# Performance work log

Hardware: AMD Instinct MI355X
Metric: run time of the kernel (lower is better)

The kernel has to match this reference:

```python
import math
import jax, jax.numpy as jnp
import numpy as np

DIM = 512
HEADS = 8
LS = 64  # local_size
SCALE = (DIM // HEADS) ** -0.5


def _normalize(x, eps=1e-12):
    # torch F.normalize(dim=-1): x / max(||x||, eps)
    n = jnp.linalg.norm(x, axis=-1, keepdims=True)
    return x / jnp.maximum(n, eps)


def setup_inputs() -> dict:
    key = jax.random.key(0)
    k0, k1, k2 = jax.random.split(key, 3)
    B, S, D = 8, 4096, DIM
    return {
        "x": jax.random.normal(k0, (B, S, D), jnp.float32),
        "W_qkv": jax.random.normal(k1, (D, 3 * D), jnp.float32) * 0.02,
        "b_qkv": jnp.zeros((3 * D,), jnp.float32),
        "W_proj": jax.random.normal(k2, (D, D), jnp.float32) * 0.02,
        "b_proj": jnp.zeros((D,), jnp.float32),
    }


def reference(x, W_qkv, b_qkv, W_proj, b_proj):
    B, S, D = x.shape
    H = HEADS
    d = D // H
    ls = LS
    nl = S // ls
    ntimes = int(math.log2(nl))

    # qkv projection -> [3, B, H, S, d]
    qkv = (x @ W_qkv + b_qkv).reshape(B, S, 3, H, d).transpose(2, 0, 3, 1, 4)
    q_pre = qkv[0].reshape(B * H, S, d).transpose(0, 2, 1)  # [BH, d, S]

    q_idx_last = jnp.broadcast_to(jnp.arange(S)[None, :], (B * H, S))

    # recursive content-based bipartition (unrolled: ntimes is static)
    for _ in range(ntimes):
        bh, dd, n = q_pre.shape
        q_avg = q_pre.reshape(bh, dd, 2, n // 2).mean(-1)        # [bh, d, 2]
        q_avg = _normalize(q_avg.transpose(0, 2, 1))             # [bh, 2, d]
        q_norm = _normalize(q_pre.transpose(0, 2, 1))            # [bh, n, d]
        # squared euclidean distance [bh, n, 2]
        sq = (jnp.sum(q_norm ** 2, -1)[:, :, None]
              + jnp.sum(q_avg ** 2, -1)[:, None, :]
              - 2.0 * jnp.einsum('bnd,bcd->bnc', q_norm, q_avg))
        q_ratio = (sq[:, :, 0] + 1.0) / (sq[:, :, 1] + 1.0)
        q_idx = jnp.argsort(q_ratio, axis=-1)                    # [bh, n]
        q_idx_last = jnp.take_along_axis(q_idx_last, q_idx, axis=-1).reshape(bh * 2, n // 2)
        q_pre = jnp.take_along_axis(q_pre, q_idx[:, None, :], axis=-1)
        # 'b d (c n) -> (b c) d n' with c=2
        q_pre = q_pre.reshape(bh, dd, 2, n // 2).transpose(0, 2, 1, 3).reshape(bh * 2, dd, n // 2)

    q_idx = q_idx_last.reshape(B, H, S)
    q_idx_rev = jnp.argsort(q_idx, axis=-1)

    # gather qkv along token dim with routed permutation
    qkv_pre = jnp.take_along_axis(qkv, q_idx[None, :, :, :, None], axis=3)  # [3,B,H,S,d]
    # 'qkv b h (nl ls) d -> qkv (b nl) h ls d'
    qkv_pre = qkv_pre.reshape(3, B, H, nl, ls, d).transpose(0, 1, 3, 2, 4, 5).reshape(3, B * nl, H, ls, d)
    q, k, v = qkv_pre[0], qkv_pre[1], qkv_pre[2]

    # windowed diff-softmax-mul attention (softmax over head dim d)
    attn = jax.nn.softmax((q - k) * SCALE, axis=-1)
    out = attn * v                                               # [(B nl), H, ls, d]

    # '(b nl) h ls d -> b h d (nl ls)'
    out = out.reshape(B, nl, H, ls, d).transpose(0, 2, 4, 1, 3).reshape(B, H, d, S)
    out = jnp.take_along_axis(out, q_idx_rev[:, :, None, :], axis=-1)
    res = out.reshape(B, D, S).transpose(0, 2, 1)                # [B, S, D]
    res = res @ W_proj + b_proj
    return x + res
```

## Files before the change

kernel.cpp:

```cpp
#include <hip/hip_runtime.h>
#include <hip/hip_bf16.h>

typedef __bf16 bf16;
typedef __attribute__((ext_vector_type(8))) __bf16 bf16x8;
typedef __attribute__((ext_vector_type(4))) __bf16 bf16x4;
typedef __attribute__((ext_vector_type(4))) float f32x4;

#define M_TOK 32768
#define D_    512
#define N_QKV 1536
#define BK    64
#define SCALE_ 0.125f

#define AS1 __attribute__((address_space(1)))
#define AS3 __attribute__((address_space(3)))

__global__ __launch_bounds__(256) void cvt_bf16(const float* __restrict__ in,
                                                bf16* __restrict__ out, int n4) {
  int i = blockIdx.x * 256 + threadIdx.x;
  if (i >= n4) return;
  f32x4 v = ((const f32x4*)in)[i];
  bf16x4 o;
  o[0] = (bf16)v[0]; o[1] = (bf16)v[1]; o[2] = (bf16)v[2]; o[3] = (bf16)v[3];
  ((bf16x4*)out)[i] = o;
}

template <int PERM>
__global__ __launch_bounds__(256) void transpose_cvt(const float* __restrict__ in,
                                                     bf16* __restrict__ out,
                                                     int K, int N) {
  __shared__ float tile[32][33];
  int n0 = blockIdx.x * 32, k0 = blockIdx.y * 32;
  int tx = threadIdx.x, ty = threadIdx.y;
  for (int i = 0; i < 32; i += 8)
    tile[ty + i][tx] = in[(size_t)(k0 + ty + i) * N + n0 + tx];
  __syncthreads();
  for (int i = 0; i < 32; i += 8) {
    int n = n0 + ty + i;
    int np = n;
    if (PERM) {
      int h = (n & 511) >> 6, qkv = n >> 9;
      np = h * 192 + qkv * 64 + (n & 63);
    }
    out[(size_t)np * K + k0 + tx] = (bf16)tile[tx][ty + i];
  }
}

__global__ __launch_bounds__(256) void gemm_qkv_softmax(const bf16* __restrict__ A,
                                                        const bf16* __restrict__ Bt,
                                                        const float* __restrict__ bqkv,
                                                        bf16* __restrict__ O) {
  __shared__ __align__(16) bf16 sA[128 * BK];
  __shared__ __align__(16) bf16 sB[192 * BK];

  const int tid = threadIdx.x;
  const int w = tid >> 6;
  const int l = tid & 63;
  const int m0 = blockIdx.x * 128;
  const int h  = blockIdx.y;
  const int n0 = h * 192;

  f32x4 acc[2][12];
#pragma unroll
  for (int i = 0; i < 2; ++i)
#pragma unroll
    for (int j = 0; j < 12; ++j) {
      f32x4 z = {0.f, 0.f, 0.f, 0.f};
      acc[i][j] = z;
    }

  const int srow = l >> 3;
  const int schunk = ((l & 7) ^ (l >> 3)) * 8;

  const int fr = l & 15;
  const int fkc = l >> 4;
  const int frs = fr & 7;

  for (int kt = 0; kt < D_; kt += BK) {
#pragma unroll
    for (int q = 0; q < 4; ++q) {
      int rowb = w * 32 + q * 8;
      const bf16* gp = A + (size_t)(m0 + rowb + srow) * D_ + kt + schunk;
      __builtin_amdgcn_global_load_lds((AS1 void*)gp, (AS3 void*)&sA[rowb * BK], 16, 0, 0);
    }
#pragma unroll
    for (int q = 0; q < 6; ++q) {
      int rowb = w * 48 + q * 8;
      const bf16* gp = Bt + (size_t)(n0 + rowb + srow) * D_ + kt + schunk;
      __builtin_amdgcn_global_load_lds((AS1 void*)gp, (AS3 void*)&sB[rowb * BK], 16, 0, 0);
    }
    __syncthreads();

#pragma unroll
    for (int kk = 0; kk < 2; ++kk) {
      const int sw = (((kk << 2) | fkc) ^ frs) * 8;
      bf16x8 af0 = *(const bf16x8*)&sA[(w * 32 + 0  + fr) * BK + sw];
      bf16x8 af1 = *(const bf16x8*)&sA[(w * 32 + 16 + fr) * BK + sw];
#pragma unroll
      for (int j = 0; j < 12; ++j) {
        bf16x8 bfj = *(const bf16x8*)&sB[(j * 16 + fr) * BK + sw];
        acc[0][j] = __builtin_amdgcn_mfma_f32_16x16x32_bf16(af0, bfj, acc[0][j], 0, 0, 0);
        acc[1][j] = __builtin_amdgcn_mfma_f32_16x16x32_bf16(af1, bfj, acc[1][j], 0, 0, 0);
      }
    }
    __syncthreads();
  }

  float bq[4], bk[4], bv[4];
#pragma unroll
  for (int jq = 0; jq < 4; ++jq) {
    int c = h * 64 + jq * 16 + fr;
    bq[jq] = bqkv[c];
    bk[jq] = bqkv[512 + c];
    bv[jq] = bqkv[1024 + c];
  }

  const int rbase = (l >> 4) * 4;
#pragma unroll
  for (int i = 0; i < 2; ++i) {
#pragma unroll
    for (int r = 0; r < 4; ++r) {
      float sc[4];
#pragma unroll
      for (int jq = 0; jq < 4; ++jq)
        sc[jq] = (acc[i][jq][r] + bq[jq] - acc[i][jq + 4][r] - bk[jq]) * SCALE_;
      float mx = fmaxf(fmaxf(sc[0], sc[1]), fmaxf(sc[2], sc[3]));
#pragma unroll
      for (int off = 1; off < 16; off <<= 1) mx = fmaxf(mx, __shfl_xor(mx, off));
      float e[4];
      float sum = 0.f;
#pragma unroll
      for (int jq = 0; jq < 4; ++jq) { e[jq] = __expf(sc[jq] - mx); sum += e[jq]; }
#pragma unroll
      for (int off = 1; off < 16; off <<= 1) sum += __shfl_xor(sum, off);
      float inv = 1.0f / sum;
      int m = m0 + w * 32 + i * 16 + rbase + r;
#pragma unroll
      for (int jq = 0; jq < 4; ++jq) {
        float o = e[jq] * inv * (acc[i][jq + 8][r] + bv[jq]);
        O[(size_t)m * D_ + h * 64 + jq * 16 + fr] = (bf16)o;
      }
    }
  }
}

__global__ __launch_bounds__(256) void gemm_bt_f32(const bf16* __restrict__ A,
                                                   const bf16* __restrict__ Bt,
                                                   const float* __restrict__ bias,
                                                   const float* __restrict__ resid,
                                                   float* __restrict__ C,
                                                   int M, int N, int K) {
  __shared__ __align__(16) bf16 sA[128 * BK];
  __shared__ __align__(16) bf16 sB[128 * BK];

  const int tid = threadIdx.x;
  const int w = tid >> 6;
  const int l = tid & 63;
  const int m0 = blockIdx.x * 128;
  const int n0 = blockIdx.y * 128;
  const int wrow = w >> 1, wcol = w & 1;

  f32x4 acc[4][4];
#pragma unroll
  for (int i = 0; i < 4; ++i)
#pragma unroll
    for (int j = 0; j < 4; ++j) {
      f32x4 z = {0.f, 0.f, 0.f, 0.f};
      acc[i][j] = z;
    }

  const int srow = l >> 3;
  const int schunk = ((l & 7) ^ (l >> 3)) * 8;
  const int fr = l & 15;
  const int fkc = l >> 4;
  const int frs = fr & 7;

  for (int kt = 0; kt < K; kt += BK) {
#pragma unroll
    for (int q = 0; q < 4; ++q) {
      int rowb = w * 32 + q * 8;
      const bf16* gp = A + (size_t)(m0 + rowb + srow) * K + kt + schunk;
      __builtin_amdgcn_global_load_lds((AS1 void*)gp, (AS3 void*)&sA[rowb * BK], 16, 0, 0);
    }
#pragma unroll
    for (int q = 0; q < 4; ++q) {
      int rowb = w * 32 + q * 8;
      const bf16* gp = Bt + (size_t)(n0 + rowb + srow) * K + kt + schunk;
      __builtin_amdgcn_global_load_lds((AS1 void*)gp, (AS3 void*)&sB[rowb * BK], 16, 0, 0);
    }
    __syncthreads();

#pragma unroll
    for (int kk = 0; kk < 2; ++kk) {
      const int sw = (((kk << 2) | fkc) ^ frs) * 8;
      bf16x8 af[4], bfr[4];
#pragma unroll
      for (int i = 0; i < 4; ++i)
        af[i] = *(const bf16x8*)&sA[(wrow * 64 + i * 16 + fr) * BK + sw];
#pragma unroll
      for (int j = 0; j < 4; ++j)
        bfr[j] = *(const bf16x8*)&sB[(wcol * 64 + j * 16 + fr) * BK + sw];
#pragma unroll
      for (int i = 0; i < 4; ++i)
#pragma unroll
        for (int j = 0; j < 4; ++j)
          acc[i][j] = __builtin_amdgcn_mfma_f32_16x16x32_bf16(af[i], bfr[j], acc[i][j], 0, 0, 0);
    }
    __syncthreads();
  }

  const int col = l & 15;
  const int rbase = (l >> 4) * 4;
#pragma unroll
  for (int j = 0; j < 4; ++j) {
    int n = n0 + wcol * 64 + j * 16 + col;
    float bv = bias[n];
#pragma unroll
    for (int i = 0; i < 4; ++i) {
#pragma unroll
      for (int r = 0; r < 4; ++r) {
        int m = m0 + wrow * 64 + i * 16 + rbase + r;
        C[(size_t)m * N + n] = acc[i][j][r] + bv + resid[(size_t)m * N + n];
      }
    }
  }
}

extern "C" void kernel_launch(void* const* d_in, const int* in_sizes, int n_in,
                              void* d_out, int out_size, void* d_ws, size_t ws_size,
                              hipStream_t stream) {
  const float* x     = (const float*)d_in[0];
  const float* Wqkv  = (const float*)d_in[1];
  const float* bqkv  = (const float*)d_in[2];
  const float* Wproj = (const float*)d_in[3];
  const float* bproj = (const float*)d_in[4];
  float* out = (float*)d_out;

  char* ws = (char*)d_ws;
  bf16* Wq_t = (bf16*)ws;
  bf16* Wp_t = (bf16*)(ws + (size_t)N_QKV * D_ * 2);
  char* p = ws + (size_t)N_QKV * D_ * 2 + (size_t)D_ * D_ * 2;
  bf16* Xb = (bf16*)p;
  bf16* O  = (bf16*)(p + (size_t)M_TOK * D_ * 2);

  transpose_cvt<1><<<dim3(N_QKV / 32, D_ / 32), dim3(32, 8), 0, stream>>>(Wqkv, Wq_t, D_, N_QKV);
  transpose_cvt<0><<<dim3(D_ / 32, D_ / 32), dim3(32, 8), 0, stream>>>(Wproj, Wp_t, D_, D_);

  cvt_bf16<<<(M_TOK * D_ / 4 + 255) / 256, 256, 0, stream>>>(x, Xb, M_TOK * D_ / 4);

  gemm_qkv_softmax<<<dim3(M_TOK / 128, 8), 256, 0, stream>>>(Xb, Wq_t, bqkv, O);

  gemm_bt_f32<<<dim3(M_TOK / 128, D_ / 128), 256, 0, stream>>>(
      O, Wp_t, bproj, x, out, M_TOK, D_, D_);
}
```

Measured before the change: 235.2 us.

## Fuse x conversion, QKV GEMM, softmax and projection into one kernel

```diff
diff --git a/kernel.cpp b/kernel.cpp
--- a/kernel.cpp
+++ b/kernel.cpp
@@ -8,221 +8,245 @@
 
 #define M_TOK 32768
 #define D_    512
-#define N_QKV 1536
-#define BK    64
 #define SCALE_ 0.125f
 
 #define AS1 __attribute__((address_space(1)))
 #define AS3 __attribute__((address_space(3)))
 
-__global__ __launch_bounds__(256) void cvt_bf16(const float* __restrict__ in,
-                                                bf16* __restrict__ out, int n4) {
-  int i = blockIdx.x * 256 + threadIdx.x;
-  if (i >= n4) return;
-  f32x4 v = ((const f32x4*)in)[i];
-  bf16x4 o;
-  o[0] = (bf16)v[0]; o[1] = (bf16)v[1]; o[2] = (bf16)v[2]; o[3] = (bf16)v[3];
-  ((bf16x4*)out)[i] = o;
-}
-
-template <int PERM>
-__global__ __launch_bounds__(256) void transpose_cvt(const float* __restrict__ in,
-                                                     bf16* __restrict__ out,
-                                                     int K, int N) {
+__global__ __launch_bounds__(256) void transpose_cvt_all(const float* __restrict__ Wqkv,
+                                                         const float* __restrict__ Wproj,
+                                                         bf16* __restrict__ Wq_t,
+                                                         bf16* __restrict__ Wp_t) {
   __shared__ float tile[32][33];
-  int n0 = blockIdx.x * 32, k0 = blockIdx.y * 32;
-  int tx = threadIdx.x, ty = threadIdx.y;
+  const int bx = blockIdx.x;
+  const float* in;
+  bf16* out;
+  int N, n0;
+  bool perm;
+  if (bx < 48) { in = Wqkv;  out = Wq_t; N = 1536; n0 = bx * 32;        perm = true;  }
+  else         { in = Wproj; out = Wp_t; N = 512;  n0 = (bx - 48) * 32; perm = false; }
+  const int k0 = blockIdx.y * 32;
+  const int tx = threadIdx.x, ty = threadIdx.y;
   for (int i = 0; i < 32; i += 8)
     tile[ty + i][tx] = in[(size_t)(k0 + ty + i) * N + n0 + tx];
   __syncthreads();
   for (int i = 0; i < 32; i += 8) {
     int n = n0 + ty + i;
     int np = n;
-    if (PERM) {
-      int h = (n & 511) >> 6, qkv = n >> 9;
-      np = h * 192 + qkv * 64 + (n & 63);
-    }
-    out[(size_t)np * K + k0 + tx] = (bf16)tile[tx][ty + i];
+    if (perm) {
+      int qkv = n >> 9, h = (n & 511) >> 6, c = n & 63;
+      np = h * 192 + (c >> 4) * 48 + qkv * 16 + (c & 15);
+    }
+    out[(size_t)np * D_ + k0 + tx] = (bf16)tile[tx][ty + i];
   }
 }
 
-__global__ __launch_bounds__(256) void gemm_qkv_softmax(const bf16* __restrict__ A,
-                                                        const bf16* __restrict__ Bt,
-                                                        const float* __restrict__ bqkv,
-                                                        bf16* __restrict__ O) {
-  __shared__ __align__(16) bf16 sA[128 * BK];
-  __shared__ __align__(16) bf16 sB[192 * BK];
+__global__ __launch_bounds__(512, 2) void fused_attn(const float* __restrict__ x,
+                                                     const bf16* __restrict__ Wq_t,
+                                                     const float* __restrict__ bqkv,
+                                                     const bf16* __restrict__ Wp_t,
+                                                     const float* __restrict__ bproj,
+                                                     float* __restrict__ out) {
+  __shared__ __align__(16) bf16 sX[64 * 512];
+  __shared__ __align__(16) bf16 sY[2][512 * 32];
+  __shared__ __align__(16) float sS[64 * 4];
 
   const int tid = threadIdx.x;
-  const int w = tid >> 6;
-  const int l = tid & 63;
-  const int m0 = blockIdx.x * 128;
-  const int h  = blockIdx.y;
-  const int n0 = h * 192;
-
-  f32x4 acc[2][12];
+  const int w = tid >> 6, l = tid & 63;
+  const int wrow = w >> 2, wcol = w & 3;
+  const int m0 = blockIdx.x * 64;
+  const int fr = l & 15, fkc = l >> 4, frs = fr & 7;
+  const int rbase = fkc * 4;
+
+#pragma unroll
+  for (int q = 0; q < 8; ++q) {
+    int u = tid + 512 * q;
+    int row = u >> 6, slot = u & 63;
+    int gch = (slot & 56) | ((slot & 7) ^ (row & 7));
+    const float* gp = x + (size_t)(m0 + row) * D_ + gch * 8;
+    f32x4 a = *(const f32x4*)gp;
+    f32x4 b = *(const f32x4*)(gp + 4);
+    bf16x8 v;
+#pragma unroll
+    for (int e = 0; e < 4; ++e) { v[e] = (bf16)a[e]; v[4 + e] = (bf16)b[e]; }
+    *(bf16x8*)&sX[row * 512 + slot * 8] = v;
+  }
+
+  const int bsrow = tid >> 3;
+  const int bgch  = (tid & 7) ^ (bsrow & 7);
+  auto stageB = [&](int buf, int T) {
+    const int hh = T >> 3, tt = T & 7;
+#pragma unroll
+    for (int q = 0; q < 3; ++q) {
+      int row = 64 * q + bsrow;
+      const bf16* gp = Wq_t + (size_t)(hh * 192 + row) * D_ + tt * 64 + bgch * 8;
+      __builtin_amdgcn_global_load_lds((AS1 const void*)gp,
+                                       (AS3 void*)&sY[buf][4096 * q + w * 512], 16, 0, 0);
+    }
+  };
+
+  f32x4 acc[2][3];
+  auto qkvK = [&](int buf, int tt, int kk) {
+    const int cb = tt * 8 + kk * 4 + fkc;
+    const int xslot = (cb & 56) | ((cb & 7) ^ frs);
+    bf16x8 af[2], bfr[3];
+#pragma unroll
+    for (int i = 0; i < 2; ++i)
+      af[i] = *(const bf16x8*)&sX[(wrow * 32 + i * 16 + fr) * 512 + xslot * 8];
+    const int c2 = kk * 4 + fkc;
+#pragma unroll
+    for (int j = 0; j < 3; ++j)
+      bfr[j] = *(const bf16x8*)&sY[buf][(wcol * 48 + j * 16 + fr) * 64 + (c2 ^ frs) * 8];
+    __builtin_amdgcn_s_setprio(1);
+#pragma unroll
+    for (int i = 0; i < 2; ++i)
+#pragma unroll
+      for (int j = 0; j < 3; ++j)
+        acc[i][j] = __builtin_amdgcn_mfma_f32_16x16x32_bf16(af[i], bfr[j], acc[i][j], 0, 0, 0);
+    __builtin_amdgcn_s_setprio(0);
+  };
+
+  bf16x4 opk[8][2];
+
+  stageB(0, 0);
+  asm volatile("s_waitcnt lgkmcnt(0)" ::: "memory");
+
+#pragma unroll
+  for (int h = 0; h < 8; ++h) {
+#pragma unroll
+    for (int i = 0; i < 2; ++i)
+#pragma unroll
+      for (int j = 0; j < 3; ++j) {
+        f32x4 z = {0.f, 0.f, 0.f, 0.f};
+        acc[i][j] = z;
+      }
+#pragma unroll 2
+    for (int t = 0; t < 8; ++t) {
+      const int T = h * 8 + t;
+      const int buf = t & 1;
+      if (T < 63) {
+        stageB(buf ^ 1, T + 1);
+        asm volatile("s_waitcnt vmcnt(3)" ::: "memory");
+      } else {
+        asm volatile("s_waitcnt vmcnt(0)" ::: "memory");
+      }
+      __builtin_amdgcn_s_barrier();
+      qkvK(buf, t, 0);
+      qkvK(buf, t, 1);
+      if (t == 7) {
+        const int hcol = h * 64 + wcol * 16 + fr;
+        const float bq = bqkv[hcol];
+        const float bk = bqkv[512 + hcol];
+        const float bv = bqkv[1024 + hcol];
+        float ev[2][4];
+#pragma unroll
+        for (int i = 0; i < 2; ++i)
+#pragma unroll
+          for (int r = 0; r < 4; ++r) {
+            float e = __expf((acc[i][0][r] + bq - acc[i][1][r] - bk) * SCALE_);
+            ev[i][r] = e;
+            float sm = e;
+#pragma unroll
+            for (int off = 1; off < 16; off <<= 1) sm += __shfl_xor(sm, off);
+            if (fr == 0)
+              sS[(wrow * 32 + i * 16 + rbase + r) * 4 + wcol] = sm;
+          }
+        asm volatile("s_waitcnt lgkmcnt(0)" ::: "memory");
+        __builtin_amdgcn_s_barrier();
+#pragma unroll
+        for (int i = 0; i < 2; ++i) {
+          bf16x4 p;
+#pragma unroll
+          for (int r = 0; r < 4; ++r) {
+            f32x4 sv = *(const f32x4*)&sS[(wrow * 32 + i * 16 + rbase + r) * 4];
+            float tot = (sv[0] + sv[1]) + (sv[2] + sv[3]);
+            p[r] = (bf16)(ev[i][r] / tot * (acc[i][2][r] + bv));
+          }
+          opk[h][i] = p;
+        }
+      }
+      __builtin_amdgcn_s_barrier();
+    }
+  }
+
+  const int psrow = tid >> 2;
+  const int pgch  = (tid & 3) ^ (psrow & 3);
+  auto stageP = [&](int buf, int tk) {
+#pragma unroll
+    for (int q = 0; q < 4; ++q) {
+      int row = 128 * q + psrow;
+      const bf16* gp = Wp_t + (size_t)row * D_ + tk * 32 + pgch * 8;
+      __builtin_amdgcn_global_load_lds((AS1 const void*)gp,
+                                       (AS3 void*)&sY[buf][4096 * q + w * 512], 16, 0, 0);
+    }
+  };
+  stageP(0, 0);
+#pragma unroll
+  for (int h = 0; h < 8; ++h)
+#pragma unroll
+    for (int i = 0; i < 2; ++i)
+#pragma unroll
+      for (int r = 0; r < 4; ++r) {
+        int row = wrow * 32 + i * 16 + rbase + r;
+        int col = h * 64 + wcol * 16 + fr;
+        int c = col >> 3;
+        int slot = (c & 56) | ((c & 7) ^ (row & 7));
+        sX[row * 512 + slot * 8 + (col & 7)] = opk[h][i][r];
+      }
+  asm volatile("s_waitcnt lgkmcnt(0)" ::: "memory");
+  __builtin_amdgcn_s_barrier();
+
+  f32x4 pacc[2][8];
 #pragma unroll
   for (int i = 0; i < 2; ++i)
 #pragma unroll
-    for (int j = 0; j < 12; ++j) {
+    for (int j = 0; j < 8; ++j) {
       f32x4 z = {0.f, 0.f, 0.f, 0.f};
-      acc[i][j] = z;
-    }
-
-  const int srow = l >> 3;
-  const int schunk = ((l & 7) ^ (l >> 3)) * 8;
-
-  const int fr = l & 15;
-  const int fkc = l >> 4;
-  const int frs = fr & 7;
-
-  for (int kt = 0; kt < D_; kt += BK) {
-#pragma unroll
-    for (int q = 0; q < 4; ++q) {
-      int rowb = w * 32 + q * 8;
-      const bf16* gp = A + (size_t)(m0 + rowb + srow) * D_ + kt + schunk;
-      __builtin_amdgcn_global_load_lds((AS1 void*)gp, (AS3 void*)&sA[rowb * BK], 16, 0, 0);
-    }
-#pragma unroll
-    for (int q = 0; q < 6; ++q) {
-      int rowb = w * 48 + q * 8;
-      const bf16* gp = Bt + (size_t)(n0 + rowb + srow) * D_ + kt + schunk;
-      __builtin_amdgcn_global_load_lds((AS1 void*)gp, (AS3 void*)&sB[rowb * BK], 16, 0, 0);
-    }
-    __syncthreads();
-
-#pragma unroll
-    for (int kk = 0; kk < 2; ++kk) {
-      const int sw = (((kk << 2) | fkc) ^ frs) * 8;
-      bf16x8 af0 = *(const bf16x8*)&sA[(w * 32 + 0  + fr) * BK + sw];
-      bf16x8 af1 = *(const bf16x8*)&sA[(w * 32 + 16 + fr) * BK + sw];
-#pragma unroll
-      for (int j = 0; j < 12; ++j) {
-        bf16x8 bfj = *(const bf16x8*)&sB[(j * 16 + fr) * BK + sw];
-        acc[0][j] = __builtin_amdgcn_mfma_f32_16x16x32_bf16(af0, bfj, acc[0][j], 0, 0, 0);
-        acc[1][j] = __builtin_amdgcn_mfma_f32_16x16x32_bf16(af1, bfj, acc[1][j], 0, 0, 0);
-      }
-    }
-    __syncthreads();
-  }
-
-  float bq[4], bk[4], bv[4];
-#pragma unroll
-  for (int jq = 0; jq < 4; ++jq) {
-    int c = h * 64 + jq * 16 + fr;
-    bq[jq] = bqkv[c];
-    bk[jq] = bqkv[512 + c];
-    bv[jq] = bqkv[1024 + c];
-  }
-
-  const int rbase = (l >> 4) * 4;
-#pragma unroll
-  for (int i = 0; i < 2; ++i) {
-#pragma unroll
-    for (int r = 0; r < 4; ++r) {
-      float sc[4];
-#pragma unroll
-      for (int jq = 0; jq < 4; ++jq)
-        sc[jq] = (acc[i][jq][r] + bq[jq] - acc[i][jq + 4][r] - bk[jq]) * SCALE_;
-      float mx = fmaxf(fmaxf(sc[0], sc[1]), fmaxf(sc[2], sc[3]));
-#pragma unroll
-      for (int off = 1; off < 16; off <<= 1) mx = fmaxf(mx, __shfl_xor(mx, off));
-      float e[4];
-      float sum = 0.f;
-#pragma unroll
-      for (int jq = 0; jq < 4; ++jq) { e[jq] = __expf(sc[jq] - mx); sum += e[jq]; }
-#pragma unroll
-      for (int off = 1; off < 16; off <<= 1) sum += __shfl_xor(sum, off);
-      float inv = 1.0f / sum;
-      int m = m0 + w * 32 + i * 16 + rbase + r;
-#pragma unroll
-      for (int jq = 0; jq < 4; ++jq) {
-        float o = e[jq] * inv * (acc[i][jq + 8][r] + bv[jq]);
-        O[(size_t)m * D_ + h * 64 + jq * 16 + fr] = (bf16)o;
-      }
-    }
-  }
-}
-
-__global__ __launch_bounds__(256) void gemm_bt_f32(const bf16* __restrict__ A,
-                                                   const bf16* __restrict__ Bt,
-                                                   const float* __restrict__ bias,
-                                                   const float* __restrict__ resid,
-                                                   float* __restrict__ C,
-                                                   int M, int N, int K) {
-  __shared__ __align__(16) bf16 sA[128 * BK];
-  __shared__ __align__(16) bf16 sB[128 * BK];
-
-  const int tid = threadIdx.x;
-  const int w = tid >> 6;
-  const int l = tid & 63;
-  const int m0 = blockIdx.x * 128;
-  const int n0 = blockIdx.y * 128;
-  const int wrow = w >> 1, wcol = w & 1;
-
-  f32x4 acc[4][4];
-#pragma unroll
-  for (int i = 0; i < 4; ++i)
-#pragma unroll
-    for (int j = 0; j < 4; ++j) {
-      f32x4 z = {0.f, 0.f, 0.f, 0.f};
-      acc[i][j] = z;
-    }
-
-  const int srow = l >> 3;
-  const int schunk = ((l & 7) ^ (l >> 3)) * 8;
-  const int fr = l & 15;
-  const int fkc = l >> 4;
-  const int frs = fr & 7;
-
-  for (int kt = 0; kt < K; kt += BK) {
-#pragma unroll
-    for (int q = 0; q < 4; ++q) {
-      int rowb = w * 32 + q * 8;
-      const bf16* gp = A + (size_t)(m0 + rowb + srow) * K + kt + schunk;
-      __builtin_amdgcn_global_load_lds((AS1 void*)gp, (AS3 void*)&sA[rowb * BK], 16, 0, 0);
-    }
-#pragma unroll
-    for (int q = 0; q < 4; ++q) {
-      int rowb = w * 32 + q * 8;
-      const bf16* gp = Bt + (size_t)(n0 + rowb + srow) * K + kt + schunk;
-      __builtin_amdgcn_global_load_lds((AS1 void*)gp, (AS3 void*)&sB[rowb * BK], 16, 0, 0);
-    }
-    __syncthreads();
-
-#pragma unroll
-    for (int kk = 0; kk < 2; ++kk) {
-      const int sw = (((kk << 2) | fkc) ^ frs) * 8;
-      bf16x8 af[4], bfr[4];
-#pragma unroll
-      for (int i = 0; i < 4; ++i)
-        af[i] = *(const bf16x8*)&sA[(wrow * 64 + i * 16 + fr) * BK + sw];
-#pragma unroll
-      for (int j = 0; j < 4; ++j)
-        bfr[j] = *(const bf16x8*)&sB[(wcol * 64 + j * 16 + fr) * BK + sw];
-#pragma unroll
-      for (int i = 0; i < 4; ++i)
-#pragma unroll
-        for (int j = 0; j < 4; ++j)
-          acc[i][j] = __builtin_amdgcn_mfma_f32_16x16x32_bf16(af[i], bfr[j], acc[i][j], 0, 0, 0);
-    }
-    __syncthreads();
-  }
-
-  const int col = l & 15;
-  const int rbase = (l >> 4) * 4;
-#pragma unroll
-  for (int j = 0; j < 4; ++j) {
-    int n = n0 + wcol * 64 + j * 16 + col;
-    float bv = bias[n];
-#pragma unroll
-    for (int i = 0; i < 4; ++i) {
+      pacc[i][j] = z;
+    }
+
+#pragma unroll 2
+  for (int tk = 0; tk < 16; ++tk) {
+    const int buf = tk & 1;
+    if (tk < 15) {
+      stageP(buf ^ 1, tk + 1);
+      asm volatile("s_waitcnt vmcnt(4)" ::: "memory");
+    } else {
+      asm volatile("s_waitcnt vmcnt(0)" ::: "memory");
+    }
+    __builtin_amdgcn_s_barrier();
+    const int cg = tk * 4 + fkc;
+    const int xslot = (cg & 56) | ((cg & 7) ^ frs);
+    bf16x8 paf[2], pbf[8];
+#pragma unroll
+    for (int i = 0; i < 2; ++i)
+      paf[i] = *(const bf16x8*)&sX[(wrow * 32 + i * 16 + fr) * 512 + xslot * 8];
+#pragma unroll
+    for (int j = 0; j < 8; ++j) {
+      int row = wcol * 128 + j * 16 + fr;
+      pbf[j] = *(const bf16x8*)&sY[buf][row * 32 + (fkc ^ (fr & 3)) * 8];
+    }
+    __builtin_amdgcn_s_setprio(1);
+#pragma unroll
+    for (int i = 0; i < 2; ++i)
+#pragma unroll
+      for (int j = 0; j < 8; ++j)
+        pacc[i][j] = __builtin_amdgcn_mfma_f32_16x16x32_bf16(paf[i], pbf[j], pacc[i][j], 0, 0, 0);
+    __builtin_amdgcn_s_setprio(0);
+    __builtin_amdgcn_s_barrier();
+  }
+
+#pragma unroll
+  for (int j = 0; j < 8; ++j) {
+    int n = wcol * 128 + j * 16 + fr;
+    float bb = bproj[n];
+#pragma unroll
+    for (int i = 0; i < 2; ++i)
 #pragma unroll
       for (int r = 0; r < 4; ++r) {
-        int m = m0 + wrow * 64 + i * 16 + rbase + r;
-        C[(size_t)m * N + n] = acc[i][j][r] + bv + resid[(size_t)m * N + n];
-      }
-    }
+        int m = m0 + wrow * 32 + i * 16 + rbase + r;
+        out[(size_t)m * D_ + n] = pacc[i][j][r] + bb + x[(size_t)m * D_ + n];
+      }
   }
 }
 
@@ -238,18 +262,9 @@
 
   char* ws = (char*)d_ws;
   bf16* Wq_t = (bf16*)ws;
-  bf16* Wp_t = (bf16*)(ws + (size_t)N_QKV * D_ * 2);
-  char* p = ws + (size_t)N_QKV * D_ * 2 + (size_t)D_ * D_ * 2;
-  bf16* Xb = (bf16*)p;
-  bf16* O  = (bf16*)(p + (size_t)M_TOK * D_ * 2);
-
-  transpose_cvt<1><<<dim3(N_QKV / 32, D_ / 32), dim3(32, 8), 0, stream>>>(Wqkv, Wq_t, D_, N_QKV);
-  transpose_cvt<0><<<dim3(D_ / 32, D_ / 32), dim3(32, 8), 0, stream>>>(Wproj, Wp_t, D_, D_);
-
-  cvt_bf16<<<(M_TOK * D_ / 4 + 255) / 256, 256, 0, stream>>>(x, Xb, M_TOK * D_ / 4);
-
-  gemm_qkv_softmax<<<dim3(M_TOK / 128, 8), 256, 0, stream>>>(Xb, Wq_t, bqkv, O);
-
-  gemm_bt_f32<<<dim3(M_TOK / 128, D_ / 128), 256, 0, stream>>>(
-      O, Wp_t, bproj, x, out, M_TOK, D_, D_);
+  bf16* Wp_t = (bf16*)(ws + (size_t)1536 * D_ * 2);
+
+  transpose_cvt_all<<<dim3(64, 16), dim3(32, 8), 0, stream>>>(Wqkv, Wproj, Wq_t, Wp_t);
+
+  fused_attn<<<dim3(M_TOK / 64), dim3(512), 0, stream>>>(x, Wq_t, bqkv, Wp_t, bproj, out);
 }
```

After: 281.2 us. +19.6%, slower.
